# Kernel tuning notes

Measured on AMD Instinct MI355X. Metric: run time of the kernel, lower is better.

The kernel has to match this reference:

```python
import jax, jax.numpy as jnp
import numpy as np
from functools import partial

H = 2048      # hidden_size
DI = 4096     # intermediate_size
N = 16        # ssm_state_size
K = 4         # conv_kernel_size
R = 128       # time_step_rank
B = 2
L = 1024


def setup_inputs() -> dict:
    key = jax.random.key(0)
    ks = jax.random.split(key, 10)
    s = 0.02
    return {
        "x": jax.random.normal(ks[0], (B, L, H), jnp.float32),
        "Win": jax.random.normal(ks[1], (2 * DI, H), jnp.float32) * s,      # in_proj weight
        "Wconv": jax.random.normal(ks[2], (DI, 1, K), jnp.float32) * 0.2,   # depthwise conv weight
        "bconv": jax.random.normal(ks[3], (DI,), jnp.float32) * 0.1,
        "Wx": jax.random.normal(ks[4], (R + 2 * N, DI), jnp.float32) * s,   # x_proj weight (no bias)
        "Wdt": jax.random.normal(ks[5], (DI, R), jnp.float32) * s,          # dt_proj weight
        "bdt": jax.random.normal(ks[6], (DI,), jnp.float32) * 0.1,
        "Wout": jax.random.normal(ks[7], (H, DI), jnp.float32) * s,         # out_proj weight (no bias)
        "A_log": jnp.log(jnp.broadcast_to(jnp.arange(1, N + 1, dtype=jnp.float32), (DI, N))),
        "D": jnp.ones((DI,), jnp.float32),
    }


def _silu(v):
    return v * jax.nn.sigmoid(v)


def _mamba_fwd(x, Win, Wconv, bconv, Wx, Wdt, bdt, Wout, A_log, D):
    sg = jax.lax.stop_gradient
    # in_proj -> [B, 2*DI, L]
    proj = jnp.einsum('blh,eh->bel', x, Win)
    hs, gate = proj[:, :DI], proj[:, DI:]          # [B, DI, L] each
    # depthwise causal conv1d, left pad K-1, trimmed to seq_len
    hs = jax.lax.conv_general_dilated(
        hs, Wconv, window_strides=(1,), padding=[(K - 1, 0)],
        dimension_numbers=('NCH', 'OIH', 'NCH'), feature_group_count=DI)
    hs = _silu(hs + bconv[None, :, None])          # [B, DI, L]
    # x_proj on [B, L, DI]
    ssm_p = jnp.einsum('bdl,pd->blp', hs, Wx)      # [B, L, R+2N]
    dt_in, Bm, Cm = ssm_p[..., :R], ssm_p[..., R:R + N], ssm_p[..., R + N:]
    dt = jax.nn.softplus(jnp.einsum('blr,dr->bld', dt_in, Wdt) + bdt)  # [B, L, DI]
    dt = jnp.transpose(dt, (0, 2, 1))              # [B, DI, L]
    A = -jnp.exp(A_log)                            # [DI, N]
    dA = jnp.exp(A[None, :, None, :] * dt[:, :, :, None])              # [B, DI, L, N]
    dBu = sg(dt[:, :, :, None] * Bm[:, None, :, :]) * hs[:, :, :, None]
    dA = sg(dA)
    Cm = sg(Cm)
    # sequential selective scan over time
    xs = (jnp.transpose(dA, (2, 0, 1, 3)),         # [L, B, DI, N]
          jnp.transpose(dBu, (2, 0, 1, 3)),
          jnp.transpose(Cm, (1, 0, 2)))            # [L, B, N]
    h0 = jnp.zeros((x.shape[0], DI, N), jnp.float32)

    def step(h, inp):
        dA_t, dBu_t, C_t = inp
        h = dA_t * h + dBu_t
        y = jnp.einsum('bdn,bn->bd', h, C_t)
        return h, y

    _, ys = jax.lax.scan(step, h0, xs)             # ys: [L, B, DI]
    y = jnp.transpose(ys, (1, 2, 0))               # [B, DI, L]
    y = y + hs * D[None, :, None]
    y = y * _silu(gate)
    y = y / 2.0 + sg(y / 2.0)                      # gradient-halving trick (fwd-identity)
    return jnp.einsum('bdl,hd->blh', y, Wout)      # [B, L, H]


def reference(x, Win, Wconv, bconv, Wx, Wdt, bdt, Wout, A_log, D):
    return _mamba_fwd(x, Win, Wconv, bconv, Wx, Wdt, bdt, Wout, A_log, D)
```

## Files before the change

kernel.cpp:

```cpp
#include <hip/hip_runtime.h>
#include <hip/hip_bf16.h>

#define HH 2048
#define DI 4096
#define NS 16
#define RR 128
#define NB 2
#define LL 1024
#define BL (NB*LL)
#define E2 (2*DI)
#define NPAD 256
#define NC 16
#define CL (LL/NC)
#define KSPL 8

typedef __bf16  bf16x8 __attribute__((ext_vector_type(8)));
typedef unsigned short u16x8 __attribute__((ext_vector_type(8)));
typedef unsigned short u16x4 __attribute__((ext_vector_type(4)));
typedef float   f32x4  __attribute__((ext_vector_type(4)));

__device__ __forceinline__ unsigned short f2bf(float f) {
  union { float f; unsigned u; } v; v.f = f;
  unsigned u = v.u;
  unsigned r = (u + 0x7FFFu + ((u >> 16) & 1u)) >> 16;
  return (unsigned short)r;
}
__device__ __forceinline__ float bf2f(unsigned short u) {
  union { unsigned u; float f; } v; v.u = ((unsigned)u) << 16; return v.f;
}

__device__ __forceinline__ float sigm(float x) { return 1.f / (1.f + __expf(-x)); }

__device__ __forceinline__ float softplus_hw(float v) {
  return (v > 20.f) ? v : __logf(1.f + __expf(v));
}

__device__ __forceinline__ void gload_lds16(const void* g, void* l) {
  __builtin_amdgcn_global_load_lds(
      (const __attribute__((address_space(1))) void*)g,
      (__attribute__((address_space(3))) void*)l, 16, 0, 0);
}

#define CPRE_X   ((long)BL*HH/8)
#define CPRE_WIN ((long)E2*HH/8)
#define CPRE_WX  ((long)NPAD*DI/8)
#define CPRE_WDT ((long)DI*RR/8)
__global__ void cast_pre(const float* __restrict__ x, const float* __restrict__ Win,
                         const float* __restrict__ Wx, const float* __restrict__ Wdt,
                         unsigned short* __restrict__ xb, unsigned short* __restrict__ winb,
                         unsigned short* __restrict__ wxb, unsigned short* __restrict__ wdtb) {
  const long NT = CPRE_X + CPRE_WIN + CPRE_WX + CPRE_WDT;
  long stride = (long)gridDim.x * blockDim.x;
  for (long c = (long)blockIdx.x * blockDim.x + threadIdx.x; c < NT; c += stride) {
    const float* src; unsigned short* dst; long i; bool zero = false;
    if (c < CPRE_X)                          { src = x;   dst = xb;   i = c; }
    else if (c < CPRE_X + CPRE_WIN)          { src = Win; dst = winb; i = c - CPRE_X; }
    else if (c < CPRE_X + CPRE_WIN + CPRE_WX){ src = Wx;  dst = wxb;  i = c - CPRE_X - CPRE_WIN;
                                               zero = (i >= 160L * (DI / 8)); }
    else                                     { src = Wdt; dst = wdtb; i = c - CPRE_X - CPRE_WIN - CPRE_WX; }
    u16x8 r;
    if (zero) {
      #pragma unroll
      for (int k = 0; k < 8; k++) r[k] = 0;
    } else {
      const float4* p = (const float4*)src + i * 2;
      float4 a = p[0], b = p[1];
      r[0]=f2bf(a.x); r[1]=f2bf(a.y); r[2]=f2bf(a.z); r[3]=f2bf(a.w);
      r[4]=f2bf(b.x); r[5]=f2bf(b.y); r[6]=f2bf(b.z); r[7]=f2bf(b.w);
    }
    ((u16x8*)dst)[i] = r;
  }
}

__global__ void cast8(const float* __restrict__ in, unsigned short* __restrict__ out, long n8) {
  long stride = (long)gridDim.x * blockDim.x;
  for (long c = (long)blockIdx.x * blockDim.x + threadIdx.x; c < n8; c += stride) {
    const float4* p = (const float4*)in + c * 2;
    float4 a = p[0], b = p[1];
    u16x8 r;
    r[0]=f2bf(a.x); r[1]=f2bf(a.y); r[2]=f2bf(a.z); r[3]=f2bf(a.w);
    r[4]=f2bf(b.x); r[5]=f2bf(b.y); r[6]=f2bf(b.z); r[7]=f2bf(b.w);
    ((u16x8*)out)[c] = r;
  }
}

__global__ __launch_bounds__(512, 1) void gemm1_256(
    const unsigned short* __restrict__ A, const unsigned short* __restrict__ Bm,
    unsigned short* __restrict__ Chs, float* __restrict__ Cgate)
{
  __shared__ unsigned short lds[8 * 8192];

  const int tid  = threadIdx.x;
  const int lane = tid & 63;
  const int wid  = tid >> 6;
  const int mBlk = blockIdx.y * 256;
  const int nBlk = blockIdx.x * 256;
  const int wm = (wid >> 2) * 128;
  const int wn = (wid & 3) * 64;

  const int sr  = tid >> 2;
  const int sc  = tid & 3;
  const int scl = sc ^ ((sr >> 1) & 3);
  const unsigned short* gA = A  + (size_t)(mBlk + sr) * HH + scl * 8;
  const unsigned short* gB = Bm + (size_t)(nBlk + sr) * HH + scl * 8;

#define LDSH(mat, buf, kh) (lds + (((mat)*2 + (buf))*2 + (kh)) * 8192)
#define STG(mat, kt, kh)                                                     \
  {                                                                          \
    const unsigned short* g_ = ((mat) ? gB : gA) + (kt) * 64 + (kh) * 32;    \
    unsigned short* l_ = LDSH(mat, (kt) & 1, kh);                            \
    gload_lds16(g_,                    l_ + tid * 8);                        \
    gload_lds16(g_ + (size_t)128 * HH, l_ + 4096 + tid * 8);                 \
  }

  const int fr = lane & 15;
  const int fq = lane >> 4;
  const int sw = fq ^ ((fr >> 1) & 3);

  f32x4 acc[8][4];
  #pragma unroll
  for (int i = 0; i < 8; i++)
    #pragma unroll
    for (int j = 0; j < 4; j++) {
      acc[i][j][0]=0.f; acc[i][j][1]=0.f; acc[i][j][2]=0.f; acc[i][j][3]=0.f;
    }

  const int nt = HH / 64;

  STG(0,0,0); STG(1,0,0); STG(0,0,1); STG(1,0,1); STG(0,1,0); STG(1,1,0);
  asm volatile("s_waitcnt vmcnt(4)" ::: "memory");
  __builtin_amdgcn_s_barrier();
  __builtin_amdgcn_sched_barrier(0);

  bf16x8 af[8], bg[2];

#define READ_AF(p, kh)                                                        \
  _Pragma("unroll")                                                           \
  for (int i = 0; i < 8; i++)                                                 \
    af[i] = *(const bf16x8*)(LDSH(0, p, kh) + (wm + i*16 + fr)*32 + sw*8);
#define READ_BG(p, h, kh)                                                     \
  bg[0] = *(const bf16x8*)(LDSH(1, p, kh) + (wn + (2*(h)  )*16 + fr)*32 + sw*8); \
  bg[1] = *(const bf16x8*)(LDSH(1, p, kh) + (wn + (2*(h)+1)*16 + fr)*32 + sw*8);
#define MFMA_PH(h)                                                            \
  __builtin_amdgcn_s_setprio(1);                                              \
  _Pragma("unroll")                                                           \
  for (int i = 0; i < 8; i++) {                                               \
    acc[i][2*(h)  ] = __builtin_amdgcn_mfma_f32_16x16x32_bf16(af[i], bg[0], acc[i][2*(h)  ], 0,0,0); \
    acc[i][2*(h)+1] = __builtin_amdgcn_mfma_f32_16x16x32_bf16(af[i], bg[1], acc[i][2*(h)+1], 0,0,0); \
  }                                                                           \
  __builtin_amdgcn_s_setprio(0);
#define BAR() __builtin_amdgcn_s_barrier(); __builtin_amdgcn_sched_barrier(0);

  for (int t = 0; t < nt; ++t) {
    const int p = t & 1;
    READ_AF(p, 0); READ_BG(p, 0, 0);
    if (t + 1 < nt) STG(0, t + 1, 1);
    BAR(); MFMA_PH(0); BAR();
    READ_BG(p, 1, 0);
    if (t + 1 < nt) STG(1, t + 1, 1);
    BAR(); MFMA_PH(1); BAR();
    READ_AF(p, 1); READ_BG(p, 0, 1);
    if (t + 2 < nt) STG(0, t + 2, 0);
    BAR(); MFMA_PH(0); BAR();
    READ_BG(p, 1, 1);
    if (t + 2 < nt) {
      STG(1, t + 2, 0);
      asm volatile("s_waitcnt vmcnt(4)" ::: "memory");
    } else {
      asm volatile("s_waitcnt vmcnt(0)" ::: "memory");
    }
    BAR(); MFMA_PH(1); BAR();
  }

  const int cr = fq * 4;
  #pragma unroll
  for (int i = 0; i < 8; i++)
    #pragma unroll
    for (int j = 0; j < 4; j++) {
      int col = nBlk + wn + j * 16 + fr;
      #pragma unroll
      for (int r = 0; r < 4; r++) {
        int row = mBlk + wm + i * 16 + cr + r;
        float v = acc[i][j][r];
        if (nBlk < DI) Chs[(size_t)row * DI + col] = f2bf(v);
        else           Cgate[(size_t)row * DI + (col - DI)] = v;
      }
    }
#undef LDSH
#undef STG
#undef READ_AF
#undef READ_BG
#undef MFMA_PH
#undef BAR
}

template<int EPI>
__global__ __launch_bounds__(256, 2) void gemm_nt(
    const unsigned short* __restrict__ A, const unsigned short* __restrict__ B,
    float* __restrict__ C, int K, int lda, int ldb, int ldc,
    const float* __restrict__ bias)
{
  __shared__ unsigned short As[128 * 32];
  __shared__ unsigned short Bs[128 * 32];

  const int tid  = threadIdx.x;
  const int lane = tid & 63;
  const int wid  = tid >> 6;
  const int mBlk = blockIdx.y * 128;
  const int nBlk = blockIdx.x * 128;
  const int wm = (wid >> 1) * 64;
  const int wn = (wid & 1) * 64;

  const int srow = wid * 32 + (lane >> 2);
  const int sk   = (lane & 3) * 8;
  const unsigned short* ga0 = A + (size_t)(mBlk + srow) * lda + sk;
  const unsigned short* ga1 = A + (size_t)(mBlk + srow + 16) * lda + sk;
  const unsigned short* gb0 = B + (size_t)(nBlk + srow) * ldb + sk;
  const unsigned short* gb1 = B + (size_t)(nBlk + srow + 16) * ldb + sk;
  unsigned short* la0 = &As[(wid * 32) * 32];
  unsigned short* la1 = &As[(wid * 32 + 16) * 32];
  unsigned short* lb0 = &Bs[(wid * 32) * 32];
  unsigned short* lb1 = &Bs[(wid * 32 + 16) * 32];

  const int fr = lane & 15;
  const int fq = lane >> 4;

  f32x4 acc[4][4];
  #pragma unroll
  for (int i = 0; i < 4; i++)
    #pragma unroll
    for (int j = 0; j < 4; j++) {
      acc[i][j][0] = 0.f; acc[i][j][1] = 0.f; acc[i][j][2] = 0.f; acc[i][j][3] = 0.f;
    }

  for (int k0 = 0; k0 < K; k0 += 32) {
    __syncthreads();
    gload_lds16(ga0 + k0, la0);
    gload_lds16(ga1 + k0, la1);
    gload_lds16(gb0 + k0, lb0);
    gload_lds16(gb1 + k0, lb1);
    __syncthreads();
    bf16x8 af[4], bg[4];
    #pragma unroll
    for (int i = 0; i < 4; i++) {
      af[i] = *(const bf16x8*)&As[(wm + i * 16 + fr) * 32 + fq * 8];
      bg[i] = *(const bf16x8*)&Bs[(wn + i * 16 + fr) * 32 + fq * 8];
    }
    #pragma unroll
    for (int i = 0; i < 4; i++)
      #pragma unroll
      for (int j = 0; j < 4; j++)
        acc[i][j] = __builtin_amdgcn_mfma_f32_16x16x32_bf16(af[i], bg[j], acc[i][j], 0, 0, 0);
  }

  const int cr = (lane >> 4) * 4;
  const int cc = lane & 15;
  #pragma unroll
  for (int i = 0; i < 4; i++)
    #pragma unroll
    for (int j = 0; j < 4; j++) {
      int col = nBlk + wn + j * 16 + cc;
      float bb = (EPI == 1) ? bias[col] : 0.f;
      #pragma unroll
      for (int r = 0; r < 4; r++) {
        int row = mBlk + wm + i * 16 + cr + r;
        float v = acc[i][j][r];
        if (EPI == 1) v = softplus_hw(v + bb);
        C[(size_t)row * ldc + col] = v;
      }
    }
}

__global__ __launch_bounds__(256, 2) void gemm_nt_64(
    const unsigned short* __restrict__ A, const unsigned short* __restrict__ B,
    float* __restrict__ C, int K, int lda, int ldb, int ldc)
{
  __shared__ unsigned short As[128 * 32];
  __shared__ unsigned short Bs[64 * 32];

  const int tid  = threadIdx.x;
  const int lane = tid & 63;
  const int wid  = tid >> 6;
  const int mBlk = blockIdx.y * 128;
  const int nBlk = blockIdx.x * 64;
  const int wm = (wid >> 1) * 64;
  const int wn = (wid & 1) * 32;

  const int srow = lane >> 2;
  const int sk   = (lane & 3) * 8;
  const unsigned short* ga0 = A + (size_t)(mBlk + wid * 32 + srow) * lda + sk;
  const unsigned short* ga1 = ga0 + (size_t)16 * lda;
  const unsigned short* gb  = B + (size_t)(nBlk + wid * 16 + srow) * ldb + sk;
  unsigned short* la0 = &As[(wid * 32) * 32];
  unsigned short* la1 = &As[(wid * 32 + 16) * 32];
  unsigned short* lb  = &Bs[(wid * 16) * 32];

  const int fr = lane & 15;
  const int fq = lane >> 4;

  f32x4 acc[4][2];
  #pragma unroll
  for (int i = 0; i < 4; i++)
    #pragma unroll
    for (int j = 0; j < 2; j++) {
      acc[i][j][0] = 0.f; acc[i][j][1] = 0.f; acc[i][j][2] = 0.f; acc[i][j][3] = 0.f;
    }

  for (int k0 = 0; k0 < K; k0 += 32) {
    __syncthreads();
    gload_lds16(ga0 + k0, la0);
    gload_lds16(ga1 + k0, la1);
    gload_lds16(gb  + k0, lb);
    __syncthreads();
    bf16x8 af[4], bg[2];
    #pragma unroll
    for (int i = 0; i < 4; i++)
      af[i] = *(const bf16x8*)&As[(wm + i * 16 + fr) * 32 + fq * 8];
    #pragma unroll
    for (int j = 0; j < 2; j++)
      bg[j] = *(const bf16x8*)&Bs[(wn + j * 16 + fr) * 32 + fq * 8];
    #pragma unroll
    for (int i = 0; i < 4; i++)
      #pragma unroll
      for (int j = 0; j < 2; j++)
        acc[i][j] = __builtin_amdgcn_mfma_f32_16x16x32_bf16(af[i], bg[j], acc[i][j], 0, 0, 0);
  }

  const int cr = (lane >> 4) * 4;
  const int cc = lane & 15;
  #pragma unroll
  for (int i = 0; i < 4; i++)
    #pragma unroll
    for (int j = 0; j < 2; j++) {
      int col = nBlk + wn + j * 16 + cc;
      #pragma unroll
      for (int r = 0; r < 4; r++) {
        int row = mBlk + wm + i * 16 + cr + r;
        C[(size_t)row * ldc + col] = acc[i][j][r];
      }
    }
}

__global__ __launch_bounds__(256, 2) void gemm_nt_splitk(
    const unsigned short* __restrict__ A, const unsigned short* __restrict__ B,
    float* __restrict__ part, int K, int lda, int ldb)
{
  __shared__ unsigned short As[128 * 32];
  __shared__ unsigned short Bs[128 * 32];

  const int tid  = threadIdx.x;
  const int lane = tid & 63;
  const int wid  = tid >> 6;
  const int mBlk = blockIdx.y * 128;
  const int nBlk = blockIdx.x * 128;
  const int kBeg = blockIdx.z * (K / KSPL);
  const int kEnd = kBeg + K / KSPL;
  const int wm = (wid >> 1) * 64;
  const int wn = (wid & 1) * 64;

  const int srow = wid * 32 + (lane >> 2);
  const int sk   = (lane & 3) * 8;
  const unsigned short* ga0 = A + (size_t)(mBlk + srow) * lda + sk;
  const unsigned short* ga1 = A + (size_t)(mBlk + srow + 16) * lda + sk;
  const unsigned short* gb0 = B + (size_t)(nBlk + srow) * ldb + sk;
  const unsigned short* gb1 = B + (size_t)(nBlk + srow + 16) * ldb + sk;
  unsigned short* la0 = &As[(wid * 32) * 32];
  unsigned short* la1 = &As[(wid * 32 + 16) * 32];
  unsigned short* lb0 = &Bs[(wid * 32) * 32];
  unsigned short* lb1 = &Bs[(wid * 32 + 16) * 32];

  const int fr = lane & 15;
  const int fq = lane >> 4;

  f32x4 acc[4][4];
  #pragma unroll
  for (int i = 0; i < 4; i++)
    #pragma unroll
    for (int j = 0; j < 4; j++) {
      acc[i][j][0] = 0.f; acc[i][j][1] = 0.f; acc[i][j][2] = 0.f; acc[i][j][3] = 0.f;
    }

  for (int k0 = kBeg; k0 < kEnd; k0 += 32) {
    __syncthreads();
    gload_lds16(ga0 + k0, la0);
    gload_lds16(ga1 + k0, la1);
    gload_lds16(gb0 + k0, lb0);
    gload_lds16(gb1 + k0, lb1);
    __syncthreads();
    bf16x8 af[4], bg[4];
    #pragma unroll
    for (int i = 0; i < 4; i++) {
      af[i] = *(const bf16x8*)&As[(wm + i * 16 + fr) * 32 + fq * 8];
      bg[i] = *(const bf16x8*)&Bs[(wn + i * 16 + fr) * 32 + fq * 8];
    }
    #pragma unroll
    for (int i = 0; i < 4; i++)
      #pragma unroll
      for (int j = 0; j < 4; j++)
        acc[i][j] = __builtin_amdgcn_mfma_f32_16x16x32_bf16(af[i], bg[j], acc[i][j], 0, 0, 0);
  }

  float* Cz = part + (size_t)blockIdx.z * BL * NPAD;
  const int cr = (lane >> 4) * 4;
  const int cc = lane & 15;
  #pragma unroll
  for (int i = 0; i < 4; i++)
    #pragma unroll
    for (int j = 0; j < 4; j++) {
      int col = nBlk + wn + j * 16 + cc;
      #pragma unroll
      for (int r = 0; r < 4; r++) {
        int row = mBlk + wm + i * 16 + cr + r;
        Cz[(size_t)row * NPAD + col] = acc[i][j][r];
      }
    }
}

__global__ __launch_bounds__(256) void reduce_ssmp(
    const float* __restrict__ part, float* __restrict__ ssmp,
    unsigned short* __restrict__ dtin)
{
  int idx = blockIdx.x * 256 + threadIdx.x;
  int row = idx >> 6;
  int c4  = (idx & 63) * 4;
  f32x4 s = {0.f, 0.f, 0.f, 0.f};
  #pragma unroll
  for (int z = 0; z < KSPL; z++) {
    f32x4 v = *(const f32x4*)(part + (size_t)z * BL * NPAD + (size_t)row * NPAD + c4);
    s[0] += v[0]; s[1] += v[1]; s[2] += v[2]; s[3] += v[3];
  }
  *(f32x4*)(ssmp + (size_t)row * NPAD + c4) = s;
  if (c4 < RR) {
    u16x4 r;
    r[0] = f2bf(s[0]); r[1] = f2bf(s[1]); r[2] = f2bf(s[2]); r[3] = f2bf(s[3]);
    *(u16x4*)(dtin + (size_t)row * RR + c4) = r;
  }
}

__global__ __launch_bounds__(256) void conv_silu(
    const unsigned short* __restrict__ ph, const float* __restrict__ Wconv,
    const float* __restrict__ bconv, unsigned short* __restrict__ hs_b)
{
  const int d   = blockIdx.x * 256 + threadIdx.x;
  const int bl0 = blockIdx.y * 8;
  const int b   = bl0 >> 10;
  const int l0  = bl0 & 1023;
  const float w0 = Wconv[d * 4 + 0], w1 = Wconv[d * 4 + 1];
  const float w2 = Wconv[d * 4 + 2], w3 = Wconv[d * 4 + 3];
  const float bc = bconv[d];
  float in[11];
  #pragma unroll
  for (int i = 0; i < 11; i++) {
    int l = l0 - 3 + i;
    in[i] = (l < 0) ? 0.f : bf2f(ph[(size_t)(b * 1024 + l) * DI + d]);
  }
  #pragma unroll
  for (int j = 0; j < 8; j++) {
    float v = in[j] * w0 + in[j + 1] * w1 + in[j + 2] * w2 + in[j + 3] * w3 + bc;
    v = v * sigm(v);
    hs_b[(size_t)(bl0 + j) * DI + d] = f2bf(v);
  }
}

template<int PASS>
__global__ __launch_bounds__(256) void scan_chunk(
    const float* __restrict__ ssm_p, const float* __restrict__ dt_t,
    const unsigned short* __restrict__ hs_b, const float* __restrict__ gate_f,
    const float* __restrict__ A_log, const float* __restrict__ Dv,
    float* __restrict__ summ, const float* __restrict__ h0buf,
    unsigned short* __restrict__ y_b)
{
  const int d = blockIdx.x * 256 + threadIdx.x;
  const int c = blockIdx.y;
  const int b = blockIdx.z;
  float Ac[16];
  #pragma unroll
  for (int n = 0; n < 16; n++) Ac[n] = -__expf(A_log[d * 16 + n]);
  const float Dd = Dv[d];
  float h[16], P[16];
  if (PASS == 0) {
    #pragma unroll
    for (int n = 0; n < 16; n++) { h[n] = 0.f; P[n] = 1.f; }
  } else {
    #pragma unroll
    for (int n = 0; n < 16; n++)
      h[n] = h0buf[((size_t)(b * NC + c) * 16 + n) * DI + d];
  }
  const float* sp = ssm_p + ((size_t)b * LL + c * CL) * NPAD;
  const size_t bl0 = (size_t)b * LL + c * CL;
  for (int l = 0; l < CL; ++l) {
    size_t bl = bl0 + l;
    float dt = dt_t[bl * DI + d];
    float hs = bf2f(hs_b[bl * DI + d]);
    float u = dt * hs;
    float y = 0.f;
    #pragma unroll
    for (int n = 0; n < 16; n++) {
      float dA = __expf(Ac[n] * dt);
      float Bn = sp[l * NPAD + 128 + n];
      h[n] = dA * h[n] + u * Bn;
      if (PASS == 0) P[n] *= dA;
      else           y += h[n] * sp[l * NPAD + 144 + n];
    }
    if (PASS == 1) {
      float gate = gate_f[bl * DI + d];
      float yy = (y + hs * Dd) * gate * sigm(gate);
      y_b[bl * DI + d] = f2bf(yy);
    }
  }
  if (PASS == 0) {
    #pragma unroll
    for (int n = 0; n < 16; n++) {
      summ[((size_t)(b * NC + c) * 32 + n)      * DI + d] = P[n];
      summ[((size_t)(b * NC + c) * 32 + 16 + n) * DI + d] = h[n];
    }
  }
}

__global__ __launch_bounds__(256) void scan_combine(
    const float* __restrict__ summ, float* __restrict__ h0buf)
{
  int idx = blockIdx.x * 256 + threadIdx.x;
  int d = idx & (DI - 1);
  int rest = idx >> 12;
  int n = rest & 15;
  int b = rest >> 4;
  float h = 0.f;
  for (int c = 0; c < NC; c++) {
    h0buf[((size_t)(b * NC + c) * 16 + n) * DI + d] = h;
    float Pv = summ[((size_t)(b * NC + c) * 32 + n)      * DI + d];
    float Hv = summ[((size_t)(b * NC + c) * 32 + 16 + n) * DI + d];
    h = Pv * h + Hv;
  }
}

extern "C" void kernel_launch(void* const* d_in, const int* in_sizes, int n_in,
                              void* d_out, int out_size, void* d_ws, size_t ws_size,
                              hipStream_t stream) {
  const float* x     = (const float*)d_in[0];
  const float* Win   = (const float*)d_in[1];
  const float* Wconv = (const float*)d_in[2];
  const float* bconv = (const float*)d_in[3];
  const float* Wx    = (const float*)d_in[4];
  const float* Wdt   = (const float*)d_in[5];
  const float* bdt   = (const float*)d_in[6];
  const float* Wout  = (const float*)d_in[7];
  const float* A_log = (const float*)d_in[8];
  const float* Dv    = (const float*)d_in[9];
  float* out = (float*)d_out;

  char* ws = (char*)d_ws;
  size_t o = 0;
  auto take = [&](size_t sz) { char* p = ws + o; o += (sz + 255) & ~(size_t)255; return p; };

  unsigned short* ph_b   = (unsigned short*)take((size_t)BL * DI * 2);
  float*          gate_f = (float*)         take((size_t)BL * DI * 4);
  unsigned short* hs_b   = (unsigned short*)take((size_t)BL * DI * 2);
  float*          ssmp   = (float*)         take((size_t)BL * NPAD * 4);
  unsigned short* dtin   = (unsigned short*)take((size_t)BL * RR * 2);
  float*          dt_t   = (float*)         take((size_t)BL * DI * 4);
  unsigned short* wxb    = (unsigned short*)take((size_t)NPAD * DI * 2);
  unsigned short* wdtb   = (unsigned short*)take((size_t)DI * RR * 2);
  float*          summ   = (float*)         take((size_t)NB * NC * 32 * DI * 4);
  float*          h0b    = (float*)         take((size_t)NB * NC * 16 * DI * 4);
  char* uni = take((size_t)BL * HH * 2 + (size_t)E2 * HH * 2);
  unsigned short* xb    = (unsigned short*)uni;
  unsigned short* winb  = (unsigned short*)(uni + (size_t)BL * HH * 2);
  unsigned short* woutb = (unsigned short*)uni;
  unsigned short* y_b   = (unsigned short*)(uni + (size_t)HH * DI * 2);
  float* part = summ;

  hipLaunchKernelGGL(cast_pre, dim3(2048), dim3(256), 0, stream,
                     x, Win, Wx, Wdt, xb, winb, wxb, wdtb);

  hipLaunchKernelGGL(gemm1_256, dim3(E2 / 256, BL / 256), dim3(512), 0, stream,
                     xb, winb, ph_b, gate_f);

  hipLaunchKernelGGL(cast8, dim3(2048), dim3(256), 0, stream, Wout, woutb, (long)HH * DI / 8);

  hipLaunchKernelGGL(conv_silu, dim3(DI / 256, BL / 8), dim3(256), 0, stream,
                     ph_b, Wconv, bconv, hs_b);

  hipLaunchKernelGGL(gemm_nt_splitk, dim3(NPAD / 128, BL / 128, KSPL), dim3(256), 0, stream,
                     hs_b, wxb, part, DI, DI, DI);
  hipLaunchKernelGGL(reduce_ssmp, dim3(BL * NPAD / 4 / 256), dim3(256), 0, stream,
                     part, ssmp, dtin);

  hipLaunchKernelGGL((gemm_nt<1>), dim3(DI / 128, BL / 128), dim3(256), 0, stream,
                     dtin, wdtb, dt_t, RR, RR, RR, DI, bdt);

  hipLaunchKernelGGL((scan_chunk<0>), dim3(DI / 256, NC, NB), dim3(256), 0, stream,
                     ssmp, dt_t, hs_b, gate_f, A_log, Dv, summ, h0b, y_b);
  hipLaunchKernelGGL(scan_combine, dim3(NB * NS * DI / 256), dim3(256), 0, stream, summ, h0b);
  hipLaunchKernelGGL((scan_chunk<1>), dim3(DI / 256, NC, NB), dim3(256), 0, stream,
                     ssmp, dt_t, hs_b, gate_f, A_log, Dv, summ, h0b, y_b);

  hipLaunchKernelGGL(gemm_nt_64, dim3(HH / 64, BL / 128), dim3(256), 0, stream,
                     y_b, woutb, out, DI, DI, DI, HH);
}
```

Baseline: 295.1 us.

## Store gate in bf16, fold Wout cast into pre-cast, drop sched barriers

Measured after the change: 293.0 us. About the same (-0.7%).

```diff
diff --git a/kernel.cpp b/kernel.cpp
--- a/kernel.cpp
+++ b/kernel.cpp
@@ -41,23 +41,27 @@
       (__attribute__((address_space(3))) void*)l, 16, 0, 0);
 }
 
-#define CPRE_X   ((long)BL*HH/8)
-#define CPRE_WIN ((long)E2*HH/8)
-#define CPRE_WX  ((long)NPAD*DI/8)
-#define CPRE_WDT ((long)DI*RR/8)
+#define CPRE_X    ((long)BL*HH/8)
+#define CPRE_WIN  ((long)E2*HH/8)
+#define CPRE_WX   ((long)NPAD*DI/8)
+#define CPRE_WDT  ((long)DI*RR/8)
+#define CPRE_WOUT ((long)HH*DI/8)
 __global__ void cast_pre(const float* __restrict__ x, const float* __restrict__ Win,
                          const float* __restrict__ Wx, const float* __restrict__ Wdt,
+                         const float* __restrict__ Wout,
                          unsigned short* __restrict__ xb, unsigned short* __restrict__ winb,
-                         unsigned short* __restrict__ wxb, unsigned short* __restrict__ wdtb) {
-  const long NT = CPRE_X + CPRE_WIN + CPRE_WX + CPRE_WDT;
+                         unsigned short* __restrict__ wxb, unsigned short* __restrict__ wdtb,
+                         unsigned short* __restrict__ woutb) {
+  const long NT = CPRE_X + CPRE_WIN + CPRE_WX + CPRE_WDT + CPRE_WOUT;
   long stride = (long)gridDim.x * blockDim.x;
   for (long c = (long)blockIdx.x * blockDim.x + threadIdx.x; c < NT; c += stride) {
     const float* src; unsigned short* dst; long i; bool zero = false;
-    if (c < CPRE_X)                          { src = x;   dst = xb;   i = c; }
-    else if (c < CPRE_X + CPRE_WIN)          { src = Win; dst = winb; i = c - CPRE_X; }
-    else if (c < CPRE_X + CPRE_WIN + CPRE_WX){ src = Wx;  dst = wxb;  i = c - CPRE_X - CPRE_WIN;
-                                               zero = (i >= 160L * (DI / 8)); }
-    else                                     { src = Wdt; dst = wdtb; i = c - CPRE_X - CPRE_WIN - CPRE_WX; }
+    long c1 = c - CPRE_X, c2 = c1 - CPRE_WIN, c3 = c2 - CPRE_WX, c4 = c3 - CPRE_WDT;
+    if (c < CPRE_X)        { src = x;    dst = xb;    i = c; }
+    else if (c1 < CPRE_WIN){ src = Win;  dst = winb;  i = c1; }
+    else if (c2 < CPRE_WX) { src = Wx;   dst = wxb;   i = c2; zero = (i >= 160L * (DI / 8)); }
+    else if (c3 < CPRE_WDT){ src = Wdt;  dst = wdtb;  i = c3; }
+    else                   { src = Wout; dst = woutb; i = c4; }
     u16x8 r;
     if (zero) {
       #pragma unroll
@@ -72,21 +76,9 @@
   }
 }
 
-__global__ void cast8(const float* __restrict__ in, unsigned short* __restrict__ out, long n8) {
-  long stride = (long)gridDim.x * blockDim.x;
-  for (long c = (long)blockIdx.x * blockDim.x + threadIdx.x; c < n8; c += stride) {
-    const float4* p = (const float4*)in + c * 2;
-    float4 a = p[0], b = p[1];
-    u16x8 r;
-    r[0]=f2bf(a.x); r[1]=f2bf(a.y); r[2]=f2bf(a.z); r[3]=f2bf(a.w);
-    r[4]=f2bf(b.x); r[5]=f2bf(b.y); r[6]=f2bf(b.z); r[7]=f2bf(b.w);
-    ((u16x8*)out)[c] = r;
-  }
-}
-
 __global__ __launch_bounds__(512, 1) void gemm1_256(
     const unsigned short* __restrict__ A, const unsigned short* __restrict__ Bm,
-    unsigned short* __restrict__ Chs, float* __restrict__ Cgate)
+    unsigned short* __restrict__ Chs, unsigned short* __restrict__ Cgate)
 {
   __shared__ unsigned short lds[8 * 8192];
 
@@ -130,7 +122,6 @@
   STG(0,0,0); STG(1,0,0); STG(0,0,1); STG(1,0,1); STG(0,1,0); STG(1,1,0);
   asm volatile("s_waitcnt vmcnt(4)" ::: "memory");
   __builtin_amdgcn_s_barrier();
-  __builtin_amdgcn_sched_barrier(0);
 
   bf16x8 af[8], bg[2];
 
@@ -149,7 +140,7 @@
     acc[i][2*(h)+1] = __builtin_amdgcn_mfma_f32_16x16x32_bf16(af[i], bg[1], acc[i][2*(h)+1], 0,0,0); \
   }                                                                           \
   __builtin_amdgcn_s_setprio(0);
-#define BAR() __builtin_amdgcn_s_barrier(); __builtin_amdgcn_sched_barrier(0);
+#define BAR() __builtin_amdgcn_s_barrier();
 
   for (int t = 0; t < nt; ++t) {
     const int p = t & 1;
@@ -183,7 +174,7 @@
         int row = mBlk + wm + i * 16 + cr + r;
         float v = acc[i][j][r];
         if (nBlk < DI) Chs[(size_t)row * DI + col] = f2bf(v);
-        else           Cgate[(size_t)row * DI + (col - DI)] = v;
+        else           Cgate[(size_t)row * DI + (col - DI)] = f2bf(v);
       }
     }
 #undef LDSH
@@ -465,7 +456,7 @@
 template<int PASS>
 __global__ __launch_bounds__(256) void scan_chunk(
     const float* __restrict__ ssm_p, const float* __restrict__ dt_t,
-    const unsigned short* __restrict__ hs_b, const float* __restrict__ gate_f,
+    const unsigned short* __restrict__ hs_b, const unsigned short* __restrict__ gate_b,
     const float* __restrict__ A_log, const float* __restrict__ Dv,
     float* __restrict__ summ, const float* __restrict__ h0buf,
     unsigned short* __restrict__ y_b)
@@ -503,7 +494,7 @@
       else           y += h[n] * sp[l * NPAD + 144 + n];
     }
     if (PASS == 1) {
-      float gate = gate_f[bl * DI + d];
+      float gate = bf2f(gate_b[bl * DI + d]);
       float yy = (y + hs * Dd) * gate * sigm(gate);
       y_b[bl * DI + d] = f2bf(yy);
     }
@@ -554,29 +545,27 @@
   auto take = [&](size_t sz) { char* p = ws + o; o += (sz + 255) & ~(size_t)255; return p; };
 
   unsigned short* ph_b   = (unsigned short*)take((size_t)BL * DI * 2);
-  float*          gate_f = (float*)         take((size_t)BL * DI * 4);
+  unsigned short* gate_b = (unsigned short*)take((size_t)BL * DI * 2);
   unsigned short* hs_b   = (unsigned short*)take((size_t)BL * DI * 2);
   float*          ssmp   = (float*)         take((size_t)BL * NPAD * 4);
   unsigned short* dtin   = (unsigned short*)take((size_t)BL * RR * 2);
   float*          dt_t   = (float*)         take((size_t)BL * DI * 4);
   unsigned short* wxb    = (unsigned short*)take((size_t)NPAD * DI * 2);
   unsigned short* wdtb   = (unsigned short*)take((size_t)DI * RR * 2);
+  unsigned short* woutb  = (unsigned short*)take((size_t)HH * DI * 2);
   float*          summ   = (float*)         take((size_t)NB * NC * 32 * DI * 4);
   float*          h0b    = (float*)         take((size_t)NB * NC * 16 * DI * 4);
   char* uni = take((size_t)BL * HH * 2 + (size_t)E2 * HH * 2);
   unsigned short* xb    = (unsigned short*)uni;
   unsigned short* winb  = (unsigned short*)(uni + (size_t)BL * HH * 2);
-  unsigned short* woutb = (unsigned short*)uni;
-  unsigned short* y_b   = (unsigned short*)(uni + (size_t)HH * DI * 2);
+  unsigned short* y_b   = (unsigned short*)uni;
   float* part = summ;
 
   hipLaunchKernelGGL(cast_pre, dim3(2048), dim3(256), 0, stream,
-                     x, Win, Wx, Wdt, xb, winb, wxb, wdtb);
+                     x, Win, Wx, Wdt, Wout, xb, winb, wxb, wdtb, woutb);
 
   hipLaunchKernelGGL(gemm1_256, dim3(E2 / 256, BL / 256), dim3(512), 0, stream,
-                     xb, winb, ph_b, gate_f);
-
-  hipLaunchKernelGGL(cast8, dim3(2048), dim3(256), 0, stream, Wout, woutb, (long)HH * DI / 8);
+                     xb, winb, ph_b, gate_b);
 
   hipLaunchKernelGGL(conv_silu, dim3(DI / 256, BL / 8), dim3(256), 0, stream,
                      ph_b, Wconv, bconv, hs_b);
@@ -590,10 +579,10 @@
                      dtin, wdtb, dt_t, RR, RR, RR, DI, bdt);
 
   hipLaunchKernelGGL((scan_chunk<0>), dim3(DI / 256, NC, NB), dim3(256), 0, stream,
-                     ssmp, dt_t, hs_b, gate_f, A_log, Dv, summ, h0b, y_b);
+                     ssmp, dt_t, hs_b, gate_b, A_log, Dv, summ, h0b, y_b);
   hipLaunchKernelGGL(scan_combine, dim3(NB * NS * DI / 256), dim3(256), 0, stream, summ, h0b);
   hipLaunchKernelGGL((scan_chunk<1>), dim3(DI / 256, NC, NB), dim3(256), 0, stream,
-                     ssmp, dt_t, hs_b, gate_f, A_log, Dv, summ, h0b, y_b);
+                     ssmp, dt_t, hs_b, gate_b, A_log, Dv, summ, h0b, y_b);
 
   hipLaunchKernelGGL(gemm_nt_64, dim3(HH / 64, BL / 128), dim3(256), 0, stream,
                      y_b, woutb, out, DI, DI, DI, HH);
```
